# Performance work log

Hardware: AMD Instinct MI355X
Metric: run time of the kernel (lower is better)

Reference implementation:

```python
import jax, jax.numpy as jnp
import numpy as np

NUM_EMBED = 1024
NUM_HEADS = 16
BLOCK_SIZE = 2048


def setup_inputs() -> dict:
    key = jax.random.key(0)
    k1, k2, k3, k4, k5 = jax.random.split(key, 5)
    C = NUM_EMBED
    s = 1.0 / np.sqrt(C)
    x = jax.random.normal(k1, (2, BLOCK_SIZE, C), dtype=jnp.float32)
    # nn.Linear params: weight (out,in), bias (out,)
    w_attn = jax.random.uniform(k2, (3 * C, C), minval=-s, maxval=s, dtype=jnp.float32)
    b_attn = jax.random.uniform(k3, (3 * C,), minval=-s, maxval=s, dtype=jnp.float32)
    w_proj = jax.random.uniform(k4, (C, C), minval=-s, maxval=s, dtype=jnp.float32)
    b_proj = jax.random.uniform(k5, (C,), minval=-s, maxval=s, dtype=jnp.float32)
    return {"x": x, "w_attn": w_attn, "b_attn": b_attn, "w_proj": w_proj, "b_proj": b_proj}


def reference(x, w_attn, b_attn, w_proj, b_proj):
    B, T, C = x.shape
    H = NUM_HEADS
    D = C // H
    kqv = jnp.einsum('btc,oc->bto', x, w_attn) + b_attn  # (B,T,3C)
    # Original code splits as K, Q, V in that order.
    K, Q, V = jnp.split(kqv, 3, axis=2)
    K = K.reshape(B, T, H, D).transpose(0, 2, 1, 3)  # (B,H,T,D)
    Q = Q.reshape(B, T, H, D).transpose(0, 2, 1, 3)
    V = V.reshape(B, T, H, D).transpose(0, 2, 1, 3)
    aff = jnp.einsum('bhqd,bhkd->bhqk', Q, K) * (D ** -0.5)  # (B,H,T,T)
    causal = jnp.tril(jnp.ones((T, T), dtype=bool))
    aff = jnp.where(causal[None, None], aff, jnp.float32(-jnp.inf))
    wei = jax.nn.softmax(aff, axis=-1)
    attn = jnp.einsum('bhqk,bhkd->bhqd', wei, V)
    attn = attn.transpose(0, 2, 1, 3).reshape(B, T, C)
    out = jnp.einsum('btc,oc->bto', attn, w_proj) + b_proj
    return out
```

## Files before the change

kernel.cpp:

```cpp
#include <hip/hip_runtime.h>
#include <hip/hip_bf16.h>
#include <cstdint>

typedef __attribute__((ext_vector_type(8))) short bf16x8;
typedef __attribute__((ext_vector_type(4))) float f32x4;
typedef __attribute__((ext_vector_type(4))) uint16_t u16x4;

__device__ __forceinline__ uint16_t f2b(float f) {
  union { float f; uint32_t i; } v; v.f = f;
  return (uint16_t)((v.i + 0x7FFFu + ((v.i >> 16) & 1u)) >> 16);
}

#define GLDS16(g, l) __builtin_amdgcn_global_load_lds( \
    (const __attribute__((address_space(1))) void*)(g), \
    (__attribute__((address_space(3))) void*)(l), 16, 0, 0)

__global__ __launch_bounds__(256) void cvt_all(
    const float* __restrict__ x, const float* __restrict__ wa, const float* __restrict__ wp,
    uint16_t* __restrict__ xb, uint16_t* __restrict__ wab, uint16_t* __restrict__ wpb) {
  const int i = (blockIdx.x * 256 + threadIdx.x) * 4;
  const float* src; uint16_t* dst; int off;
  if (i < 4194304)      { src = x;  dst = xb;  off = i; }
  else if (i < 7340032) { src = wa; dst = wab; off = i - 4194304; }
  else                  { src = wp; dst = wpb; off = i - 7340032; }
  const float4 v = *(const float4*)(src + off);
  u16x4 o;
  o.x = f2b(v.x); o.y = f2b(v.y); o.z = f2b(v.z); o.w = f2b(v.w);
  *(u16x4*)(dst + off) = o;
}

template <int BM, bool OUT_BF16>
__global__ __launch_bounds__(256) void gemm_bt_bias(
    const uint16_t* __restrict__ A, const uint16_t* __restrict__ B,
    const float* __restrict__ bias, void* __restrict__ Cv,
    int M, int N, int K) {
  constexpr int MI = BM / 32;
  constexpr int CHA = BM / 16;
  constexpr int CPW = (CHA + 8) / 4;
  constexpr size_t ST_BYTES = (size_t)(BM + 128) * 32 * 2;
  constexpr size_t CT_BYTES = OUT_BF16 ? (size_t)4 * (BM / 2) * 72 * 2
                                       : (size_t)4 * (BM / 2) * 68 * 4;
  constexpr size_t LB = CT_BYTES > ST_BYTES ? CT_BYTES : ST_BYTES;
  __shared__ alignas(16) unsigned char ldsb[LB];
  uint16_t* lds = (uint16_t*)ldsb;
  const int offB = BM * 32;

  const int tid = threadIdx.x;
  const int wave = tid >> 6, lane = tid & 63;
  const int q4 = lane >> 4, l16 = lane & 15;
  const int wm = wave >> 1, wn = wave & 1;
  const long blockM = (long)blockIdx.y * BM;
  const long blockN = (long)blockIdx.x * 128;

  f32x4 acc[MI][4] = {};

  for (int k0 = 0; k0 < K; k0 += 32) {
#pragma unroll
    for (int c = 0; c < CPW; ++c) {
      const int id = c * 4 + wave;
      const bool isB = id >= CHA;
      const int a = isB ? id - CHA : id;
      const uint16_t* mat = isB ? B : A;
      const long rowBase = isB ? blockN : blockM;
      const int off = isB ? offB : 0;
      const int flat = a * 64 + lane;
      const int row = flat >> 2, seg = flat & 3;
      GLDS16(mat + (rowBase + row) * (long)K + k0 + seg * 8, lds + off + a * 512);
    }
    __syncthreads();
    bf16x8 af[MI], bfr[4];
#pragma unroll
    for (int i = 0; i < MI; ++i)
      af[i] = *(const bf16x8*)&lds[(wm * (BM / 2) + i * 16 + l16) * 32 + q4 * 8];
#pragma unroll
    for (int j = 0; j < 4; ++j)
      bfr[j] = *(const bf16x8*)&lds[offB + (wn * 64 + j * 16 + l16) * 32 + q4 * 8];
#pragma unroll
    for (int i = 0; i < MI; ++i)
#pragma unroll
      for (int j = 0; j < 4; ++j)
        acc[i][j] = __builtin_amdgcn_mfma_f32_16x16x32_bf16(af[i], bfr[j], acc[i][j], 0, 0, 0);
    __syncthreads();
  }

  if (OUT_BF16) {
    uint16_t* ct = lds + wave * (BM / 2) * 72;
#pragma unroll
    for (int j = 0; j < 4; ++j) {
      const float bv = bias[blockN + wn * 64 + j * 16 + l16];
#pragma unroll
      for (int i = 0; i < MI; ++i)
#pragma unroll
        for (int r = 0; r < 4; ++r)
          ct[(i * 16 + q4 * 4 + r) * 72 + j * 16 + l16] = f2b(acc[i][j][r] + bv);
    }
    __syncthreads();
    uint16_t* Cb = (uint16_t*)Cv;
#pragma unroll
    for (int st = 0; st < BM / 16; ++st) {
      const int flat = st * 64 + lane;
      const int row = flat >> 3, seg = flat & 7;
      const bf16x8 v = *(const bf16x8*)&ct[row * 72 + seg * 8];
      *(bf16x8*)&Cb[(blockM + wm * (BM / 2) + row) * (long)N + blockN + wn * 64 + seg * 8] = v;
    }
  } else {
    float* ct = (float*)ldsb + wave * (BM / 2) * 68;
#pragma unroll
    for (int j = 0; j < 4; ++j) {
      const float bv = bias[blockN + wn * 64 + j * 16 + l16];
#pragma unroll
      for (int i = 0; i < MI; ++i)
#pragma unroll
        for (int r = 0; r < 4; ++r)
          ct[(i * 16 + q4 * 4 + r) * 68 + j * 16 + l16] = acc[i][j][r] + bv;
    }
    __syncthreads();
    float* Cb = (float*)Cv;
#pragma unroll
    for (int st = 0; st < BM / 8; ++st) {
      const int flat = st * 64 + lane;
      const int row = flat >> 4, seg = flat & 15;
      const f32x4 v = *(const f32x4*)&ct[row * 68 + seg * 4];
      *(f32x4*)&Cb[(blockM + wm * (BM / 2) + row) * (long)N + blockN + wn * 64 + seg * 4] = v;
    }
  }
}

__global__ __launch_bounds__(256, 2) void attn_flash(
    const uint16_t* __restrict__ kqv, uint16_t* __restrict__ attn) {
  constexpr int T = 2048, C = 1024, C3 = 3072;
  __shared__ alignas(16) uint16_t Kt[128 * 72];
  __shared__ alignas(16) uint16_t Vt[64 * 136];
  __shared__ alignas(16) uint16_t Pt[4][16 * 136];
  uint32_t* VtW = (uint32_t*)Vt;

  const int tid = threadIdx.x;
  const int wave = tid >> 6, lane = tid & 63;
  const int q4 = lane >> 4, l16 = lane & 15;
  const int p = blockIdx.x >> 5, bh = blockIdx.x & 31;
  const int b = bh >> 4, h = bh & 15;
  const size_t base = (size_t)b * T * C3;
  const size_t obase = (size_t)b * T * C;
  const int hD = h * 64;
  const float sc = 0.125f * 1.4426950408889634f;

  const int qb0 = 31 - p, qb1 = p;
  const int nkt0 = (qb0 >> 1) + 1;
  const int tr = tid >> 3, kch = tid & 7;

  int qb = qb0;
  int qrow = qb * 64 + wave * 16 + l16;
  bf16x8 qf0 = *(const bf16x8*)&kqv[base + (size_t)qrow * C3 + C + hD + q4 * 8];
  bf16x8 qf1 = *(const bf16x8*)&kqv[base + (size_t)qrow * C3 + C + hD + 32 + q4 * 8];

  f32x4 o[4] = {};
  float m_i = -1e30f, l_i = 0.f;
  int kt = 0;
  bool ss1 = false;

  bf16x8 pk[4], pv[2][2];
#pragma unroll
  for (int rr = 0; rr < 4; ++rr)
    pk[rr] = *(const bf16x8*)&kqv[base + (size_t)(rr * 32 + tr) * C3 + hD + kch * 8];
#pragma unroll
  for (int s2 = 0; s2 < 2; ++s2) {
    const size_t g = base + (size_t)(2 * (s2 * 32 + tr)) * C3 + 2 * C + hD + kch * 8;
    pv[s2][0] = *(const bf16x8*)&kqv[g];
    pv[s2][1] = *(const bf16x8*)&kqv[g + C3];
  }

  uint16_t* Pw = &Pt[wave][0];

  for (int t = 0; t < 17; ++t) {
    const int kbase = kt * 128;
    const bool lastOfStrip = !ss1 ? (kt == nkt0 - 1) : (t == 16);

    __syncthreads();
#pragma unroll
    for (int rr = 0; rr < 4; ++rr)
      *(bf16x8*)&Kt[(rr * 32 + tr) * 72 + kch * 8] = pk[rr];
#pragma unroll
    for (int s2 = 0; s2 < 2; ++s2) {
      const int colw = ((s2 * 32 + tr) + 8 * kch) & 63;
      const uint32_t* a0 = (const uint32_t*)&pv[s2][0];
      const uint32_t* a1 = (const uint32_t*)&pv[s2][1];
#pragma unroll
      for (int i = 0; i < 8; ++i) {
        const uint32_t w = (i & 1)
            ? __builtin_amdgcn_perm(a1[i >> 1], a0[i >> 1], 0x07060302u)
            : __builtin_amdgcn_perm(a1[i >> 1], a0[i >> 1], 0x05040100u);
        VtW[(kch * 8 + i) * 68 + colw] = w;
      }
    }
    __syncthreads();
    if (t < 16) {
      const int kb2 = (lastOfStrip ? 0 : kt + 1) * 128;
#pragma unroll
      for (int rr = 0; rr < 4; ++rr)
        pk[rr] = *(const bf16x8*)&kqv[base + (size_t)(kb2 + rr * 32 + tr) * C3 + hD + kch * 8];
#pragma unroll
      for (int s2 = 0; s2 < 2; ++s2) {
        const size_t g = base + (size_t)(kb2 + 2 * (s2 * 32 + tr)) * C3 + 2 * C + hD + kch * 8;
        pv[s2][0] = *(const bf16x8*)&kqv[g];
        pv[s2][1] = *(const bf16x8*)&kqv[g + C3];
      }
    }
    f32x4 s[8];
#pragma unroll
    for (int nk = 0; nk < 8; ++nk) {
      f32x4 z = {};
      const bf16x8 kf0 = *(const bf16x8*)&Kt[(nk * 16 + l16) * 72 + q4 * 8];
      const bf16x8 kf1 = *(const bf16x8*)&Kt[(nk * 16 + l16) * 72 + 32 + q4 * 8];
      z = __builtin_amdgcn_mfma_f32_16x16x32_bf16(kf0, qf0, z, 0, 0, 0);
      z = __builtin_amdgcn_mfma_f32_16x16x32_bf16(kf1, qf1, z, 0, 0, 0);
      s[nk] = z;
    }
    if (kbase + 127 > qb * 64 + wave * 16) {
#pragma unroll
      for (int nk = 0; nk < 8; ++nk) {
        const int key0 = kbase + nk * 16 + q4 * 4;
#pragma unroll
        for (int r = 0; r < 4; ++r)
          s[nk][r] = (key0 + r <= qrow) ? s[nk][r] : -1e30f;
      }
    }
    float mloc = s[0][0];
#pragma unroll
    for (int nk = 0; nk < 8; ++nk)
#pragma unroll
      for (int r = 0; r < 4; ++r) mloc = fmaxf(mloc, s[nk][r]);
    mloc = fmaxf(mloc, __shfl_xor(mloc, 16, 64));
    mloc = fmaxf(mloc, __shfl_xor(mloc, 32, 64));
    const float mnew = fmaxf(m_i, mloc * sc);
    const float alpha = exp2f(m_i - mnew);
    const bool mchg = mnew > m_i;
    m_i = mnew;
    float rs = 0.f;
#pragma unroll
    for (int nk = 0; nk < 8; ++nk)
#pragma unroll
      for (int r = 0; r < 4; ++r) {
        const float pe = exp2f(fmaf(s[nk][r], sc, -mnew));
        s[nk][r] = pe;
        rs += pe;
      }
    rs += __shfl_xor(rs, 16, 64);
    rs += __shfl_xor(rs, 32, 64);
    l_i = l_i * alpha + rs;
    if (__any(mchg)) {
#pragma unroll
      for (int r = 0; r < 4; ++r) {
        const float ar = __shfl(alpha, q4 * 4 + r, 64);
#pragma unroll
        for (int d4 = 0; d4 < 4; ++d4) o[d4][r] *= ar;
      }
    }
#pragma unroll
    for (int nk = 0; nk < 8; ++nk) {
      union { __hip_bfloat162 h2; uint32_t u; } c01, c23;
      c01.h2 = __float22bfloat162_rn(make_float2(s[nk][0], s[nk][1]));
      c23.h2 = __float22bfloat162_rn(make_float2(s[nk][2], s[nk][3]));
      uint2 pkw; pkw.x = c01.u; pkw.y = c23.u;
      *(uint2*)&Pw[l16 * 136 + nk * 16 + q4 * 4] = pkw;
    }
#pragma unroll
    for (int ks = 0; ks < 4; ++ks) {
      const bf16x8 pf = *(const bf16x8*)&Pw[l16 * 136 + ks * 32 + q4 * 8];
#pragma unroll
      for (int d4 = 0; d4 < 4; ++d4) {
        const int d = d4 * 16 + l16;
        const int col = (ks * 32 + q4 * 8 + 16 * (d >> 3)) & 127;
        const bf16x8 vf = *(const bf16x8*)&Vt[d * 136 + col];
        o[d4] = __builtin_amdgcn_mfma_f32_16x16x32_bf16(pf, vf, o[d4], 0, 0, 0);
      }
    }
    if (lastOfStrip) {
      const float linv = 1.0f / l_i;
#pragma unroll
      for (int r = 0; r < 4; ++r) {
        const float lr = __shfl(linv, q4 * 4 + r, 64);
        const int q = qb * 64 + wave * 16 + q4 * 4 + r;
        const size_t rowoff = obase + (size_t)q * C + hD;
#pragma unroll
        for (int d4 = 0; d4 < 4; ++d4)
          attn[rowoff + d4 * 16 + l16] = f2b(o[d4][r] * lr);
      }
      if (!ss1) {
        ss1 = true;
        qb = qb1;
        qrow = qb * 64 + wave * 16 + l16;
        qf0 = *(const bf16x8*)&kqv[base + (size_t)qrow * C3 + C + hD + q4 * 8];
        qf1 = *(const bf16x8*)&kqv[base + (size_t)qrow * C3 + C + hD + 32 + q4 * 8];
#pragma unroll
        for (int d4 = 0; d4 < 4; ++d4) o[d4] = (f32x4){0.f, 0.f, 0.f, 0.f};
        m_i = -1e30f; l_i = 0.f;
        kt = 0;
      }
    } else {
      ++kt;
    }
  }
}

extern "C" void kernel_launch(void* const* d_in, const int* in_sizes, int n_in,
                              void* d_out, int out_size, void* d_ws, size_t ws_size,
                              hipStream_t stream) {
  const float* x      = (const float*)d_in[0];
  const float* w_attn = (const float*)d_in[1];
  const float* b_attn = (const float*)d_in[2];
  const float* w_proj = (const float*)d_in[3];
  const float* b_proj = (const float*)d_in[4];
  float* out = (float*)d_out;

  uint16_t* xb    = (uint16_t*)d_ws;
  uint16_t* wab   = xb  + (size_t)4096 * 1024;
  uint16_t* wpb   = wab + (size_t)3072 * 1024;
  uint16_t* kqv   = wpb + (size_t)1024 * 1024;
  uint16_t* attnb = kqv + (size_t)4096 * 3072;

  dim3 blk(256, 1, 1);
  hipLaunchKernelGGL(cvt_all, dim3(8192), blk, 0, stream, x, w_attn, w_proj, xb, wab, wpb);

  hipLaunchKernelGGL((gemm_bt_bias<128, true>), dim3(3072 / 128, 4096 / 128, 1), blk, 0, stream,
                     xb, wab, b_attn, (void*)kqv, 4096, 3072, 1024);
  hipLaunchKernelGGL(attn_flash, dim3(512, 1, 1), blk, 0, stream, kqv, attnb);
  hipLaunchKernelGGL((gemm_bt_bias<64, false>), dim3(1024 / 128, 4096 / 64, 1), blk, 0, stream,
                     attnb, wpb, b_proj, (void*)out, 4096, 1024, 1024);
}
```

Measured before the change: 198.9 us.

## Split attention key tile across waves with cross-wave softmax merge

Instead of each wave owning 16 query rows against all 128 keys of a tile, each wave now owns all 64 query rows against its own 32-key slice. Each wave keeps separate running max, sum and output state and rewrites its P tile into a smaller per-wave buffer. At the end of each query strip, the partial max/sum values and O accumulators are exchanged through a 64KB shared buffer and merged split-K style. The goal is to cut redundant K/V LDS fragment reads per wave, at the cost of 4x the O accumulator registers, a much larger LDS footprint that may reduce occupancy, and extra syncs at strip ends.

```diff
diff --git a/kernel.cpp b/kernel.cpp
--- a/kernel.cpp
+++ b/kernel.cpp
@@ -129,10 +129,13 @@
 __global__ __launch_bounds__(256, 2) void attn_flash(
     const uint16_t* __restrict__ kqv, uint16_t* __restrict__ attn) {
   constexpr int T = 2048, C = 1024, C3 = 3072;
-  __shared__ alignas(16) uint16_t Kt[128 * 72];
-  __shared__ alignas(16) uint16_t Vt[64 * 136];
-  __shared__ alignas(16) uint16_t Pt[4][16 * 136];
+  __shared__ alignas(16) unsigned char mainb[65536];
+  __shared__ alignas(16) float2 Sm[256];
+  uint16_t* Kt = (uint16_t*)mainb;
+  uint16_t* Vt = (uint16_t*)(mainb + 18432);
   uint32_t* VtW = (uint32_t*)Vt;
+  uint16_t* Pt = (uint16_t*)(mainb + 35840);
+  float*    Oex = (float*)mainb;
 
   const int tid = threadIdx.x;
   const int wave = tid >> 6, lane = tid & 63;
@@ -147,14 +150,21 @@
   const int qb0 = 31 - p, qb1 = p;
   const int nkt0 = (qb0 >> 1) + 1;
   const int tr = tid >> 3, kch = tid & 7;
+  const int wkb = wave * 32;
+  uint16_t* Pw = Pt + wave * 2304;
 
   int qb = qb0;
-  int qrow = qb * 64 + wave * 16 + l16;
-  bf16x8 qf0 = *(const bf16x8*)&kqv[base + (size_t)qrow * C3 + C + hD + q4 * 8];
-  bf16x8 qf1 = *(const bf16x8*)&kqv[base + (size_t)qrow * C3 + C + hD + 32 + q4 * 8];
-
-  f32x4 o[4] = {};
-  float m_i = -1e30f, l_i = 0.f;
+  bf16x8 qf[4][2];
+#pragma unroll
+  for (int ji = 0; ji < 4; ++ji) {
+    const size_t qoff = base + (size_t)(qb * 64 + ji * 16 + l16) * C3 + C + hD + q4 * 8;
+    qf[ji][0] = *(const bf16x8*)&kqv[qoff];
+    qf[ji][1] = *(const bf16x8*)&kqv[qoff + 32];
+  }
+
+  f32x4 o[4][4] = {};
+  float m_i[4] = {-1e30f, -1e30f, -1e30f, -1e30f};
+  float l_i[4] = {0.f, 0.f, 0.f, 0.f};
   int kt = 0;
   bool ss1 = false;
 
@@ -169,8 +179,6 @@
     pv[s2][1] = *(const bf16x8*)&kqv[g + C3];
   }
 
-  uint16_t* Pw = &Pt[wave][0];
-
   for (int t = 0; t < 17; ++t) {
     const int kbase = kt * 128;
     const bool lastOfStrip = !ss1 ? (kt == nkt0 - 1) : (t == 16);
@@ -205,95 +213,168 @@
         pv[s2][1] = *(const bf16x8*)&kqv[g + C3];
       }
     }
-    f32x4 s[8];
-#pragma unroll
-    for (int nk = 0; nk < 8; ++nk) {
-      f32x4 z = {};
-      const bf16x8 kf0 = *(const bf16x8*)&Kt[(nk * 16 + l16) * 72 + q4 * 8];
-      const bf16x8 kf1 = *(const bf16x8*)&Kt[(nk * 16 + l16) * 72 + 32 + q4 * 8];
-      z = __builtin_amdgcn_mfma_f32_16x16x32_bf16(kf0, qf0, z, 0, 0, 0);
-      z = __builtin_amdgcn_mfma_f32_16x16x32_bf16(kf1, qf1, z, 0, 0, 0);
-      s[nk] = z;
-    }
-    if (kbase + 127 > qb * 64 + wave * 16) {
-#pragma unroll
-      for (int nk = 0; nk < 8; ++nk) {
-        const int key0 = kbase + nk * 16 + q4 * 4;
-#pragma unroll
-        for (int r = 0; r < 4; ++r)
-          s[nk][r] = (key0 + r <= qrow) ? s[nk][r] : -1e30f;
-      }
-    }
-    float mloc = s[0][0];
-#pragma unroll
-    for (int nk = 0; nk < 8; ++nk)
-#pragma unroll
-      for (int r = 0; r < 4; ++r) mloc = fmaxf(mloc, s[nk][r]);
-    mloc = fmaxf(mloc, __shfl_xor(mloc, 16, 64));
-    mloc = fmaxf(mloc, __shfl_xor(mloc, 32, 64));
-    const float mnew = fmaxf(m_i, mloc * sc);
-    const float alpha = exp2f(m_i - mnew);
-    const bool mchg = mnew > m_i;
-    m_i = mnew;
-    float rs = 0.f;
-#pragma unroll
-    for (int nk = 0; nk < 8; ++nk)
-#pragma unroll
-      for (int r = 0; r < 4; ++r) {
-        const float pe = exp2f(fmaf(s[nk][r], sc, -mnew));
-        s[nk][r] = pe;
-        rs += pe;
-      }
-    rs += __shfl_xor(rs, 16, 64);
-    rs += __shfl_xor(rs, 32, 64);
-    l_i = l_i * alpha + rs;
+    bf16x8 kf[2][2];
+#pragma unroll
+    for (int kg = 0; kg < 2; ++kg) {
+      const uint16_t* kr = &Kt[(wkb + kg * 16 + l16) * 72 + q4 * 8];
+      kf[kg][0] = *(const bf16x8*)kr;
+      kf[kg][1] = *(const bf16x8*)(kr + 32);
+    }
+    f32x4 sv[2][4];
+#pragma unroll
+    for (int kg = 0; kg < 2; ++kg)
+#pragma unroll
+      for (int ji = 0; ji < 4; ++ji) {
+        f32x4 z = {};
+        z = __builtin_amdgcn_mfma_f32_16x16x32_bf16(kf[kg][0], qf[ji][0], z, 0, 0, 0);
+        z = __builtin_amdgcn_mfma_f32_16x16x32_bf16(kf[kg][1], qf[ji][1], z, 0, 0, 0);
+        sv[kg][ji] = z;
+      }
+#pragma unroll
+    for (int kg = 0; kg < 2; ++kg)
+#pragma unroll
+      for (int ji = 0; ji < 4; ++ji)
+#pragma unroll
+        for (int r = 0; r < 4; ++r) sv[kg][ji][r] *= sc;
+    if (kbase + 127 > qb * 64) {
+#pragma unroll
+      for (int kg = 0; kg < 2; ++kg) {
+        const int key0 = kbase + wkb + kg * 16 + q4 * 4;
+#pragma unroll
+        for (int ji = 0; ji < 4; ++ji) {
+          const int qv = qb * 64 + ji * 16 + l16;
+#pragma unroll
+          for (int r = 0; r < 4; ++r)
+            sv[kg][ji][r] = (key0 + r <= qv) ? sv[kg][ji][r] : -1e30f;
+        }
+      }
+    }
+    float alpha[4];
+    bool mchg = false;
+#pragma unroll
+    for (int ji = 0; ji < 4; ++ji) {
+      float mloc = sv[0][ji][0];
+#pragma unroll
+      for (int kg = 0; kg < 2; ++kg)
+#pragma unroll
+        for (int r = 0; r < 4; ++r) mloc = fmaxf(mloc, sv[kg][ji][r]);
+      mloc = fmaxf(mloc, __shfl_xor(mloc, 16, 64));
+      mloc = fmaxf(mloc, __shfl_xor(mloc, 32, 64));
+      const float mnew = fmaxf(m_i[ji], mloc);
+      alpha[ji] = exp2f(m_i[ji] - mnew);
+      mchg = mchg || (mnew > m_i[ji]);
+      m_i[ji] = mnew;
+      float rs = 0.f;
+#pragma unroll
+      for (int kg = 0; kg < 2; ++kg)
+#pragma unroll
+        for (int r = 0; r < 4; ++r) {
+          const float pe = exp2f(sv[kg][ji][r] - mnew);
+          sv[kg][ji][r] = pe;
+          rs += pe;
+        }
+      rs += __shfl_xor(rs, 16, 64);
+      rs += __shfl_xor(rs, 32, 64);
+      l_i[ji] = l_i[ji] * alpha[ji] + rs;
+    }
     if (__any(mchg)) {
 #pragma unroll
-      for (int r = 0; r < 4; ++r) {
-        const float ar = __shfl(alpha, q4 * 4 + r, 64);
-#pragma unroll
-        for (int d4 = 0; d4 < 4; ++d4) o[d4][r] *= ar;
-      }
-    }
-#pragma unroll
-    for (int nk = 0; nk < 8; ++nk) {
-      union { __hip_bfloat162 h2; uint32_t u; } c01, c23;
-      c01.h2 = __float22bfloat162_rn(make_float2(s[nk][0], s[nk][1]));
-      c23.h2 = __float22bfloat162_rn(make_float2(s[nk][2], s[nk][3]));
-      uint2 pkw; pkw.x = c01.u; pkw.y = c23.u;
-      *(uint2*)&Pw[l16 * 136 + nk * 16 + q4 * 4] = pkw;
-    }
-#pragma unroll
-    for (int ks = 0; ks < 4; ++ks) {
-      const bf16x8 pf = *(const bf16x8*)&Pw[l16 * 136 + ks * 32 + q4 * 8];
-#pragma unroll
-      for (int d4 = 0; d4 < 4; ++d4) {
-        const int d = d4 * 16 + l16;
-        const int col = (ks * 32 + q4 * 8 + 16 * (d >> 3)) & 127;
-        const bf16x8 vf = *(const bf16x8*)&Vt[d * 136 + col];
-        o[d4] = __builtin_amdgcn_mfma_f32_16x16x32_bf16(pf, vf, o[d4], 0, 0, 0);
-      }
+      for (int ji = 0; ji < 4; ++ji)
+#pragma unroll
+        for (int r = 0; r < 4; ++r) {
+          const float ar = __shfl(alpha[ji], q4 * 4 + r, 64);
+#pragma unroll
+          for (int dg = 0; dg < 4; ++dg) o[ji][dg][r] *= ar;
+        }
+    }
+#pragma unroll
+    for (int kg = 0; kg < 2; ++kg)
+#pragma unroll
+      for (int ji = 0; ji < 4; ++ji) {
+        union { __hip_bfloat162 h2; uint32_t u; } c01, c23;
+        c01.h2 = __float22bfloat162_rn(make_float2(sv[kg][ji][0], sv[kg][ji][1]));
+        c23.h2 = __float22bfloat162_rn(make_float2(sv[kg][ji][2], sv[kg][ji][3]));
+        uint2 pkw; pkw.x = c01.u; pkw.y = c23.u;
+        *(uint2*)&Pw[(ji * 16 + l16) * 36 + kg * 16 + q4 * 4] = pkw;
+      }
+    bf16x8 pf[4];
+#pragma unroll
+    for (int ji = 0; ji < 4; ++ji)
+      pf[ji] = *(const bf16x8*)&Pw[(ji * 16 + l16) * 36 + q4 * 8];
+#pragma unroll
+    for (int dg = 0; dg < 4; ++dg) {
+      const int d = dg * 16 + l16;
+      const int col = (wkb + q4 * 8 + 16 * (d >> 3)) & 127;
+      const bf16x8 vf = *(const bf16x8*)&Vt[d * 136 + col];
+#pragma unroll
+      for (int ji = 0; ji < 4; ++ji)
+        o[ji][dg] = __builtin_amdgcn_mfma_f32_16x16x32_bf16(pf[ji], vf, o[ji][dg], 0, 0, 0);
     }
     if (lastOfStrip) {
-      const float linv = 1.0f / l_i;
-#pragma unroll
-      for (int r = 0; r < 4; ++r) {
-        const float lr = __shfl(linv, q4 * 4 + r, 64);
-        const int q = qb * 64 + wave * 16 + q4 * 4 + r;
-        const size_t rowoff = obase + (size_t)q * C + hD;
-#pragma unroll
-        for (int d4 = 0; d4 < 4; ++d4)
-          attn[rowoff + d4 * 16 + l16] = f2b(o[d4][r] * lr);
+      if (q4 == 0) {
+#pragma unroll
+        for (int ji = 0; ji < 4; ++ji)
+          Sm[(wave * 4 + ji) * 16 + l16] = make_float2(m_i[ji], l_i[ji]);
+      }
+      __syncthreads();
+      float Lg[4], bown[4];
+#pragma unroll
+      for (int ji = 0; ji < 4; ++ji) {
+        const float2 s0 = Sm[(0 * 4 + ji) * 16 + l16];
+        const float2 s1 = Sm[(1 * 4 + ji) * 16 + l16];
+        const float2 s2 = Sm[(2 * 4 + ji) * 16 + l16];
+        const float2 s3 = Sm[(3 * 4 + ji) * 16 + l16];
+        const float M = fmaxf(fmaxf(s0.x, s1.x), fmaxf(s2.x, s3.x));
+        Lg[ji] = s0.y * exp2f(s0.x - M) + s1.y * exp2f(s1.x - M) +
+                 s2.y * exp2f(s2.x - M) + s3.y * exp2f(s3.x - M);
+        bown[ji] = exp2f(m_i[ji] - M);
+      }
+      float* myO = Oex + wave * 4096;
+#pragma unroll
+      for (int ji = 0; ji < 4; ++ji) {
+        float br[4];
+#pragma unroll
+        for (int r = 0; r < 4; ++r) br[r] = __shfl(bown[ji], q4 * 4 + r, 64);
+#pragma unroll
+        for (int dg = 0; dg < 4; ++dg) {
+          f32x4 tmp;
+#pragma unroll
+          for (int r = 0; r < 4; ++r) tmp[r] = o[ji][dg][r] * br[r];
+          *(f32x4*)&myO[(ji * 4 + dg) * 256 + lane * 4] = tmp;
+        }
+      }
+      __syncthreads();
+      float Lr[4];
+#pragma unroll
+      for (int r = 0; r < 4; ++r)
+        Lr[r] = 1.0f / __shfl(Lg[wave], q4 * 4 + r, 64);
+#pragma unroll
+      for (int dg = 0; dg < 4; ++dg) {
+        f32x4 acc = *(const f32x4*)&Oex[0 * 4096 + (wave * 4 + dg) * 256 + lane * 4];
+#pragma unroll
+        for (int w2 = 1; w2 < 4; ++w2) {
+          const f32x4 t2 = *(const f32x4*)&Oex[w2 * 4096 + (wave * 4 + dg) * 256 + lane * 4];
+#pragma unroll
+          for (int r = 0; r < 4; ++r) acc[r] += t2[r];
+        }
+#pragma unroll
+        for (int r = 0; r < 4; ++r) {
+          const int q = qb * 64 + wave * 16 + q4 * 4 + r;
+          attn[obase + (size_t)q * C + hD + dg * 16 + l16] = f2b(acc[r] * Lr[r]);
+        }
       }
       if (!ss1) {
         ss1 = true;
         qb = qb1;
-        qrow = qb * 64 + wave * 16 + l16;
-        qf0 = *(const bf16x8*)&kqv[base + (size_t)qrow * C3 + C + hD + q4 * 8];
-        qf1 = *(const bf16x8*)&kqv[base + (size_t)qrow * C3 + C + hD + 32 + q4 * 8];
-#pragma unroll
-        for (int d4 = 0; d4 < 4; ++d4) o[d4] = (f32x4){0.f, 0.f, 0.f, 0.f};
-        m_i = -1e30f; l_i = 0.f;
+#pragma unroll
+        for (int ji = 0; ji < 4; ++ji) {
+          const size_t qoff = base + (size_t)(qb * 64 + ji * 16 + l16) * C3 + C + hD + q4 * 8;
+          qf[ji][0] = *(const bf16x8*)&kqv[qoff];
+          qf[ji][1] = *(const bf16x8*)&kqv[qoff + 32];
+          m_i[ji] = -1e30f; l_i[ji] = 0.f;
+#pragma unroll
+          for (int dg = 0; dg < 4; ++dg) o[ji][dg] = (f32x4){0.f, 0.f, 0.f, 0.f};
+        }
         kt = 0;
       }
     } else {
```

New measurement: 220.3 us. 1.11x slower.
